# Kernel tuning notes

Hardware: AMD Instinct MI355X
Metric: run time of the kernel (lower is better)

Reference implementation:

```python
import jax, jax.numpy as jnp
import numpy as np

T, B, D, FF, Z = 1024, 32, 512, 2048, 64


def _trunc_normal(key, shape, std=0.001):
    return std * jax.random.truncated_normal(key, -2.0, 2.0, shape, dtype=jnp.float32)


def setup_inputs() -> dict:
    key = jax.random.key(0)
    ks = jax.random.split(key, 16)
    inp = {
        "x": jax.random.normal(ks[0], (T, B, D), dtype=jnp.float32),
        "first": jax.random.bernoulli(ks[1], 0.05, (T, B)),  # episode boundaries
        "h0": jax.random.normal(ks[2], (B, D), dtype=jnp.float32),
        "c0": jax.random.normal(ks[3], (B, D), dtype=jnp.float32),
        # pre-LN params
        "ln_g": jnp.ones((D,), jnp.float32),
        "ln_b": jnp.zeros((D,), jnp.float32),
        # LSTM params (PyTorch gate order i,f,g,o)
        "Wih": jax.random.normal(ks[4], (4 * D, D), jnp.float32) / np.sqrt(D),
        "Whh": jax.random.normal(ks[5], (4 * D, D), jnp.float32) / np.sqrt(D),
        "bih": jnp.zeros((4 * D,), jnp.float32),
        "bhh": jnp.zeros((4 * D,), jnp.float32),
        # pointwise FFN: mlp0 = Linear(D,FF)+ReLU, mlp1 = Linear(FF,D)
        "mlp0_w": jax.random.normal(ks[6], (FF, D), jnp.float32) / np.sqrt(D),
        "mlp0_b": jnp.zeros((FF,), jnp.float32),
        "mlp1_w": jax.random.normal(ks[7], (D, FF), jnp.float32) / np.sqrt(FF),
        "mlp1_b": jnp.zeros((D,), jnp.float32),
        # adapter bottleneck (trunc-normal init, std=0.001)
        "aw0": _trunc_normal(ks[8], (Z, D)),
        "ab0": _trunc_normal(ks[9], (Z,)),
        "aw1": _trunc_normal(ks[10], (D, Z)),
        "ab1": _trunc_normal(ks[11], (D,)),
    }
    return inp


def _layernorm(x, g, b, eps=1e-5):
    mu = jnp.mean(x, axis=-1, keepdims=True)
    var = jnp.mean(jnp.square(x - mu), axis=-1, keepdims=True)
    return (x - mu) * jax.lax.rsqrt(var + eps) * g + b


def _lstm_scan(x, first, h0, c0, Wih, Whh, bih, bhh):
    # x: [T,B,D], first: [T,B] bool resets state before the step
    def step(carry, inp):
        h, c = carry
        xt, ft = inp
        keep = jnp.where(ft, 0.0, 1.0)[:, None].astype(h.dtype)
        h = h * keep
        c = c * keep
        gates = xt @ Wih.T + bih + h @ Whh.T + bhh  # [B,4D]
        i, f, g, o = jnp.split(gates, 4, axis=-1)
        c = jax.nn.sigmoid(f) * c + jax.nn.sigmoid(i) * jnp.tanh(g)
        h = jax.nn.sigmoid(o) * jnp.tanh(c)
        return (h, c), h
    (h, c), ys = jax.lax.scan(step, (h0, c0), (x, first))
    return ys, h, c


def reference(x, first, h0, c0, ln_g, ln_b, Wih, Whh, bih, bhh,
              mlp0_w, mlp0_b, mlp1_w, mlp1_b, aw0, ab0, aw1, ab1):
    residual = x
    xn = _layernorm(x, ln_g, ln_b)
    y, h_out, c_out = _lstm_scan(xn, first, h0, c0, Wih, Whh, bih, bhh)
    y = y + residual  # is_residual and 'lstm' in recurrence_type
    residual = y
    # pointwise layer: mlp1(mlp0(y)) with mlp0 = Linear+ReLU
    y = jax.nn.relu(y @ mlp0_w.T + mlp0_b) @ mlp1_w.T + mlp1_b
    # adapter: y + net(y)
    y = y + jax.nn.relu(y @ aw0.T + ab0) @ aw1.T + ab1
    y = y + residual
    return (y, h_out, c_out)
```

## Files before the change

kernel.cpp:

```cpp
#include <hip/hip_runtime.h>

#define T_ 1024
#define B_ 32
#define D_ 512
#define FF_ 2048
#define TB_ 32768
#define TCH_ 512
#define RCH_ 16384

typedef short bf16x8 __attribute__((ext_vector_type(8)));
typedef float f32x4 __attribute__((ext_vector_type(4)));

static __device__ __forceinline__ unsigned int pack2bf(float a, float b){
  union { __bf16 h[2]; unsigned int u; } z;
  z.h[0] = (__bf16)a; z.h[1] = (__bf16)b; return z.u;
}
static __device__ __forceinline__ float bflo(unsigned int u){ return __uint_as_float(u<<16); }
static __device__ __forceinline__ float bfhi(unsigned int u){ return __uint_as_float(u & 0xffff0000u); }
static __device__ __forceinline__ float sigm(float x){ return 1.f/(1.f+__expf(-x)); }
static __device__ __forceinline__ float tanh_(float x){ return 1.f - 2.f/(1.f+__expf(2.f*x)); }

static __device__ __forceinline__ bool firstval(const void* p, int mode, int idx){
  return mode ? (((const int*)p)[idx] != 0) : (((const unsigned char*)p)[idx] != 0);
}

__global__ void detect_first_kernel(const unsigned char* __restrict__ p, unsigned int* __restrict__ mode){
  __shared__ int found;
  if (threadIdx.x == 0) found = 0;
  __syncthreads();
  int f = 0;
  for (int i = threadIdx.x; i < TB_; i += 256) if ((i & 3) != 0 && p[i] != 0) f = 1;
  if (f) atomicAdd(&found, 1);
  __syncthreads();
  if (threadIdx.x == 0) *mode = (found == 0) ? 1u : 0u;
}

__global__ void convert_w_kernel(const float* __restrict__ Wih, const float* __restrict__ Whh,
                                 const float* __restrict__ m0w, const float* __restrict__ m1w,
                                 const float* __restrict__ aw0, const float* __restrict__ aw1,
                                 __bf16* __restrict__ Wihb, __bf16* __restrict__ Whhb,
                                 __bf16* __restrict__ m0b,  __bf16* __restrict__ m1b,
                                 __bf16* __restrict__ awT0, __bf16* __restrict__ awT1){
  int bid = blockIdx.x;
  if (bid < 4096) {
    int ai = bid >> 10;
    size_t off = (size_t)(bid & 1023) * 1024 + threadIdx.x * 4;
    const float* src = (ai==0)?Wih:(ai==1)?Whh:(ai==2)?m0w:m1w;
    __bf16* dst = (ai==0)?Wihb:(ai==1)?Whhb:(ai==2)?m0b:m1b;
    float4 v = *(const float4*)(src + off);
    union { __bf16 h[4]; uint2 u; } z;
    z.h[0]=(__bf16)v.x; z.h[1]=(__bf16)v.y; z.h[2]=(__bf16)v.z; z.h[3]=(__bf16)v.w;
    *(uint2*)(void*)(dst + off) = z.u;
  } else {
    int e = (bid - 4096) * 256 + threadIdx.x;
    if (e < 32768) { int k = e >> 6, j = e & 63;  awT0[e] = (__bf16)aw0[j*512 + k]; }
    else { int e2 = e - 32768; int j = e2 >> 9, d = e2 & 511; awT1[e2] = (__bf16)aw1[d*64 + j]; }
  }
}

__global__ __launch_bounds__(256) void ln_kernel(const float* __restrict__ x,
                                                 const float* __restrict__ g, const float* __restrict__ b,
                                                 __bf16* __restrict__ xn){
  const int w = threadIdx.x >> 6, l = threadIdx.x & 63;
  const int row = blockIdx.x * 4 + w;
  const float* xr = x + (size_t)row * D_;
  const int e0 = l * 4, e1 = 256 + l * 4;
  float4 v0 = *(const float4*)(xr + e0);
  float4 v1 = *(const float4*)(xr + e1);
  float s  = v0.x+v0.y+v0.z+v0.w + v1.x+v1.y+v1.z+v1.w;
  float s2 = v0.x*v0.x+v0.y*v0.y+v0.z*v0.z+v0.w*v0.w + v1.x*v1.x+v1.y*v1.y+v1.z*v1.z+v1.w*v1.w;
  #pragma unroll
  for (int off = 1; off < 64; off <<= 1) { s += __shfl_xor(s, off); s2 += __shfl_xor(s2, off); }
  float mu = s * (1.f/512.f);
  float var = s2 * (1.f/512.f) - mu*mu;
  float rstd = rsqrtf(var + 1e-5f);
  float4 g0 = *(const float4*)(g + e0), g1 = *(const float4*)(g + e1);
  float4 b0 = *(const float4*)(b + e0), b1 = *(const float4*)(b + e1);
  union { __bf16 h[4]; uint2 u; } o0, o1;
  o0.h[0]=(__bf16)((v0.x-mu)*rstd*g0.x+b0.x); o0.h[1]=(__bf16)((v0.y-mu)*rstd*g0.y+b0.y);
  o0.h[2]=(__bf16)((v0.z-mu)*rstd*g0.z+b0.z); o0.h[3]=(__bf16)((v0.w-mu)*rstd*g0.w+b0.w);
  o1.h[0]=(__bf16)((v1.x-mu)*rstd*g1.x+b1.x); o1.h[1]=(__bf16)((v1.y-mu)*rstd*g1.y+b1.y);
  o1.h[2]=(__bf16)((v1.z-mu)*rstd*g1.z+b1.z); o1.h[3]=(__bf16)((v1.w-mu)*rstd*g1.w+b1.w);
  *(uint2*)(void*)(xn + (size_t)row * D_ + e0) = o0.u;
  *(uint2*)(void*)(xn + (size_t)row * D_ + e1) = o1.u;
}

template<int RELU, int BF16OUT, int TWOBIAS>
__global__ __launch_bounds__(256) void gemm_bt(const __bf16* __restrict__ A, const __bf16* __restrict__ W,
                                               const float* __restrict__ bias0, const float* __restrict__ bias1,
                                               float* __restrict__ Cf, __bf16* __restrict__ Cb,
                                               int M, int N, int K){
  __shared__ __bf16 As[128*64];
  __shared__ __bf16 Bs[128*64];
  const int tid = threadIdx.x, w = tid >> 6, l = tid & 63;
  const int bm = blockIdx.x, bn = blockIdx.y;
  const int wm = (w >> 1) * 64, wn = (w & 1) * 64;
  const int nk = K >> 6;

  uint4 ra[4], rb[4];
  #pragma unroll
  for (int i = 0; i < 4; ++i) {
    int s = tid + (i << 8); int row = s >> 3; int ks = s & 7;
    ra[i] = *(const uint4*)(void*)(A + (size_t)(bm*128 + row) * K + ks*8);
    rb[i] = *(const uint4*)(void*)(W + (size_t)(bn*128 + row) * K + ks*8);
  }
  f32x4 acc[4][4];
  #pragma unroll
  for (int mt = 0; mt < 4; ++mt)
    #pragma unroll
    for (int nt = 0; nt < 4; ++nt) acc[mt][nt] = (f32x4){0.f,0.f,0.f,0.f};

  for (int kt = 0; kt < nk; ++kt) {
    __syncthreads();
    #pragma unroll
    for (int i = 0; i < 4; ++i) {
      int s = tid + (i << 8); int row = s >> 3; int ks = s & 7;
      int wi = row * 64 + ((ks * 8) ^ ((row & 7) << 3));
      *(uint4*)(void*)(As + wi) = ra[i];
      *(uint4*)(void*)(Bs + wi) = rb[i];
    }
    __syncthreads();
    if (kt + 1 < nk) {
      #pragma unroll
      for (int i = 0; i < 4; ++i) {
        int s = tid + (i << 8); int row = s >> 3; int ks = s & 7;
        ra[i] = *(const uint4*)(void*)(A + (size_t)(bm*128 + row) * K + (kt+1)*64 + ks*8);
        rb[i] = *(const uint4*)(void*)(W + (size_t)(bn*128 + row) * K + (kt+1)*64 + ks*8);
      }
    }
    #pragma unroll
    for (int kk = 0; kk < 2; ++kk) {
      bf16x8 af[4], bfv[4];
      const int ke = kk * 32 + ((l >> 4) << 3);
      #pragma unroll
      for (int mt = 0; mt < 4; ++mt) {
        int row = wm + mt*16 + (l & 15);
        af[mt] = *(const bf16x8*)(void*)(As + row*64 + (ke ^ ((row & 7) << 3)));
      }
      #pragma unroll
      for (int nt = 0; nt < 4; ++nt) {
        int row = wn + nt*16 + (l & 15);
        bfv[nt] = *(const bf16x8*)(void*)(Bs + row*64 + (ke ^ ((row & 7) << 3)));
      }
      #pragma unroll
      for (int mt = 0; mt < 4; ++mt)
        #pragma unroll
        for (int nt = 0; nt < 4; ++nt)
          acc[mt][nt] = __builtin_amdgcn_mfma_f32_16x16x32_bf16(af[mt], bfv[nt], acc[mt][nt], 0, 0, 0);
    }
  }
  #pragma unroll
  for (int nt = 0; nt < 4; ++nt) {
    int c = bn*128 + wn + nt*16 + (l & 15);
    float bv = bias0[c];
    if (TWOBIAS) bv += bias1[c];
    #pragma unroll
    for (int mt = 0; mt < 4; ++mt) {
      #pragma unroll
      for (int j = 0; j < 4; ++j) {
        int r = bm*128 + wm + mt*16 + ((l >> 4) << 2) + j;
        float v = acc[mt][nt][j] + bv;
        if (RELU) v = fmaxf(v, 0.f);
        if (BF16OUT) Cb[(size_t)r * N + c] = (__bf16)v;
        else         Cf[(size_t)r * N + c] = v;
      }
    }
  }
}

__global__ __launch_bounds__(512) void lstm_scan(
    const __bf16* __restrict__ Whh,
    const __bf16* __restrict__ preC,
    const float*  __restrict__ x,
    const void*   __restrict__ firstp,
    const float*  __restrict__ h0,
    const float*  __restrict__ c0,
    float*        __restrict__ cstate,
    __bf16*       __restrict__ ymidbC,
    unsigned long long* __restrict__ HP,
    const unsigned int* __restrict__ modep,
    float* __restrict__ hout, float* __restrict__ cout,
    int tBase){
  const int s = blockIdx.x, tid = threadIdx.x, w = tid >> 6, l = tid & 63;
  const int d0 = s * 32;
  __shared__ __bf16 Hl[32 * 512];
  __shared__ float  gl[32 * 132];
  const int mode = (int)*modep;

  bf16x8 wf[16];
  {
    int rl = w*16 + (l & 15);
    int gr = (rl >> 5) * 512 + d0 + (rl & 31);
    const __bf16* base = Whh + (size_t)gr * 512 + ((l >> 4) << 3);
    #pragma unroll
    for (int kt = 0; kt < 16; ++kt) wf[kt] = *(const bf16x8*)(void*)(base + kt*32);
  }
  const int b = tid >> 4, dl2 = (tid & 15) * 2;
  const int dg = d0 + dl2;
  const int opid = b * 256 + s * 16 + (tid & 15);

  float cr[2];
  if (tBase == 0) {
    float k0 = firstval(firstp, mode, b) ? 0.f : 1.f;
    float2 c2 = *(const float2*)(c0 + (size_t)b*512 + dg);
    cr[0] = c2.x * k0; cr[1] = c2.y * k0;
    float2 h = *(const float2*)(h0 + (size_t)b*512 + dg);
    unsigned long long pkt = (1ULL << 32) | (unsigned long long)pack2bf(h.x*k0, h.y*k0);
    __hip_atomic_store(HP + opid, pkt, __ATOMIC_RELAXED, __HIP_MEMORY_SCOPE_AGENT);
  } else {
    float2 c2 = *(const float2*)(cstate + (size_t)b*512 + dg);
    cr[0] = c2.x; cr[1] = c2.y;
  }

  for (int tl = 0; tl < TCH_; ++tl) {
    const int t = tBase + tl;
    const int rowg = t * 32 + b, rowl = tl * 32 + b;
    unsigned int pg[4];
    #pragma unroll
    for (int gi = 0; gi < 4; ++gi)
      pg[gi] = *(const unsigned int*)(void*)(preC + (size_t)rowl * 2048 + gi*512 + dg);
    float2 xv = *(const float2*)(x + (size_t)rowg * 512 + dg);
    const bool f_t1 = (t < T_-1) ? firstval(firstp, mode, rowg + 32) : false;

    const unsigned want = (unsigned)(t + 1);
    const unsigned long long* Pb = HP + ((size_t)(t & 1) << 13);
    unsigned long long pk[16];
    #pragma unroll
    for (int j = 0; j < 16; ++j)
      pk[j] = __hip_atomic_load(Pb + tid + (j << 9), __ATOMIC_RELAXED, __HIP_MEMORY_SCOPE_AGENT);
    while (true) {
      unsigned stale = 0;
      #pragma unroll
      for (int j = 0; j < 16; ++j)
        if ((unsigned)(pk[j] >> 32) != want) stale |= (1u << j);
      if (!stale) break;
      __builtin_amdgcn_s_sleep(1);
      #pragma unroll
      for (int j = 0; j < 16; ++j)
        if (stale & (1u << j))
          pk[j] = __hip_atomic_load(Pb + tid + (j << 9), __ATOMIC_RELAXED, __HIP_MEMORY_SCOPE_AGENT);
    }
    #pragma unroll
    for (int j = 0; j < 16; ++j) {
      int pid = tid + (j << 9);
      int pb = pid >> 8, ps = (pid >> 4) & 15, pi = pid & 15;
      int q = ps*32 + pi*2;
      *(unsigned int*)(void*)(Hl + pb*512 + (q ^ ((pb & 7) << 3))) = (unsigned)pk[j];
    }
    __syncthreads();

    f32x4 a0a = (f32x4){0.f,0.f,0.f,0.f}, a0b = (f32x4){0.f,0.f,0.f,0.f};
    f32x4 a1a = (f32x4){0.f,0.f,0.f,0.f}, a1b = (f32x4){0.f,0.f,0.f,0.f};
    #pragma unroll
    for (int kt = 0; kt < 16; kt += 2) {
      int ke0 = kt*32 + ((l >> 4) << 3), ke1 = (kt+1)*32 + ((l >> 4) << 3);
      int r0 = (l & 15), r1 = 16 + (l & 15);
      bf16x8 h00 = *(const bf16x8*)(void*)(Hl + r0*512 + (ke0 ^ ((r0 & 7) << 3)));
      bf16x8 h01 = *(const bf16x8*)(void*)(Hl + r0*512 + (ke1 ^ ((r0 & 7) << 3)));
      bf16x8 h10 = *(const bf16x8*)(void*)(Hl + r1*512 + (ke0 ^ ((r1 & 7) << 3)));
      bf16x8 h11 = *(const bf16x8*)(void*)(Hl + r1*512 + (ke1 ^ ((r1 & 7) << 3)));
      a0a = __builtin_amdgcn_mfma_f32_16x16x32_bf16(h00, wf[kt],   a0a, 0, 0, 0);
      a0b = __builtin_amdgcn_mfma_f32_16x16x32_bf16(h01, wf[kt+1], a0b, 0, 0, 0);
      a1a = __builtin_amdgcn_mfma_f32_16x16x32_bf16(h10, wf[kt],   a1a, 0, 0, 0);
      a1b = __builtin_amdgcn_mfma_f32_16x16x32_bf16(h11, wf[kt+1], a1b, 0, 0, 0);
    }
    f32x4 acc0 = a0a + a0b, acc1 = a1a + a1b;
    {
      int col = w*16 + (l & 15);
      #pragma unroll
      for (int j = 0; j < 4; ++j) {
        gl[(((l >> 4) << 2) + j) * 132 + col]        = acc0[j];
        gl[((16 + ((l >> 4) << 2) + j)) * 132 + col] = acc1[j];
      }
    }
    __syncthreads();

    float2 gv[4];
    #pragma unroll
    for (int gi = 0; gi < 4; ++gi) gv[gi] = *(const float2*)(gl + b*132 + gi*32 + dl2);
    const float keep1 = f_t1 ? 0.f : 1.f;
    float hh[2], cc[2];
    #pragma unroll
    for (int p = 0; p < 2; ++p) {
      float gi_ = (p ? gv[0].y : gv[0].x) + (p ? bfhi(pg[0]) : bflo(pg[0]));
      float gf_ = (p ? gv[1].y : gv[1].x) + (p ? bfhi(pg[1]) : bflo(pg[1]));
      float gg_ = (p ? gv[2].y : gv[2].x) + (p ? bfhi(pg[2]) : bflo(pg[2]));
      float go_ = (p ? gv[3].y : gv[3].x) + (p ? bfhi(pg[3]) : bflo(pg[3]));
      float cn = sigm(gf_) * cr[p] + sigm(gi_) * tanh_(gg_);
      float h  = sigm(go_) * tanh_(cn);
      cc[p] = cn; hh[p] = h;
    }
    cr[0] = cc[0] * keep1; cr[1] = cc[1] * keep1;
    float2 yv = { hh[0] + xv.x, hh[1] + xv.y };
    if (t < T_-1) {
      unsigned long long pkt = (((unsigned long long)(unsigned)(t + 2)) << 32)
                             | (unsigned long long)pack2bf(hh[0]*keep1, hh[1]*keep1);
      __hip_atomic_store(HP + (((size_t)((t+1) & 1)) << 13) + opid, pkt,
                         __ATOMIC_RELAXED, __HIP_MEMORY_SCOPE_AGENT);
      if (tl == TCH_-1) *(float2*)(cstate + (size_t)b*512 + dg) = make_float2(cr[0], cr[1]);
    } else {
      *(float2*)(hout + (size_t)b*512 + dg) = make_float2(hh[0], hh[1]);
      *(float2*)(cout + (size_t)b*512 + dg) = make_float2(cc[0], cc[1]);
    }
    *(unsigned int*)(void*)(ymidbC + (size_t)rowl * 512 + dg) = pack2bf(yv.x, yv.y);
  }
}

__global__ __launch_bounds__(256) void adapter_out_kernel(
    float* __restrict__ y2,
    const __bf16* __restrict__ ymidb,
    const __bf16* __restrict__ awT0,
    const __bf16* __restrict__ awT1,
    const float* __restrict__ ab0, const float* __restrict__ ab1){
  __shared__ float zl[16 * 64];
  const int w = threadIdx.x >> 6, l = threadIdx.x & 63;
  const int r0 = blockIdx.x * 16;
  const float bz = ab0[l];
  #pragma unroll
  for (int rr = 0; rr < 4; ++rr) {
    int rowl = w*4 + rr;
    const float* yr = y2 + (size_t)(r0 + rowl) * 512;
    float acc = bz;
    #pragma unroll 4
    for (int k = 0; k < 512; ++k) acc += yr[k] * (float)awT0[k*64 + l];
    zl[rowl*64 + l] = fmaxf(acc, 0.f);
  }
  __syncthreads();
  #pragma unroll
  for (int rr = 0; rr < 4; ++rr) {
    int rowl = w*4 + rr; int row = r0 + rowl;
    const float* yr = y2  + (size_t)row * 512;
    const __bf16* mr = ymidb + (size_t)row * 512;
    #pragma unroll
    for (int dd = 0; dd < 8; ++dd) {
      int d = dd*64 + l;
      float acc = ab1[d] + yr[d] + (float)mr[d];
      #pragma unroll 4
      for (int j = 0; j < 64; ++j) acc += zl[rowl*64 + j] * (float)awT1[j*512 + d];
      y2[(size_t)row * 512 + d] = acc;
    }
  }
}

extern "C" void kernel_launch(void* const* d_in, const int* in_sizes, int n_in,
                              void* d_out, int out_size, void* d_ws, size_t ws_size,
                              hipStream_t stream){
  (void)in_sizes; (void)n_in; (void)out_size; (void)ws_size;
  const float* x    = (const float*)d_in[0];
  const void*  first=               d_in[1];
  const float* h0   = (const float*)d_in[2];
  const float* c0   = (const float*)d_in[3];
  const float* ln_g = (const float*)d_in[4];
  const float* ln_b = (const float*)d_in[5];
  const float* Wih  = (const float*)d_in[6];
  const float* Whh  = (const float*)d_in[7];
  const float* bih  = (const float*)d_in[8];
  const float* bhh  = (const float*)d_in[9];
  const float* m0w  = (const float*)d_in[10];
  const float* m0b  = (const float*)d_in[11];
  const float* m1w  = (const float*)d_in[12];
  const float* m1b  = (const float*)d_in[13];
  const float* aw0  = (const float*)d_in[14];
  const float* ab0  = (const float*)d_in[15];
  const float* aw1  = (const float*)d_in[16];
  const float* ab1  = (const float*)d_in[17];

  char* ws = (char*)d_ws;
  __bf16* buf0  = (__bf16*)(ws + 0LL);
  __bf16* xnbfH = (__bf16*)(ws + 67108864LL);
  __bf16* ymidbH= (__bf16*)(ws + 83886080LL);
  __bf16* wihb  = (__bf16*)(ws + 100663296LL);
  __bf16* whhb  = (__bf16*)(ws + 102760448LL);
  __bf16* m0bf  = (__bf16*)(ws + 104857600LL);
  __bf16* m1bf  = (__bf16*)(ws + 106954752LL);
  __bf16* awT0  = (__bf16*)(ws + 109051904LL);
  __bf16* awT1  = (__bf16*)(ws + 109117440LL);
  unsigned long long* HP = (unsigned long long*)(ws + 109182976LL);
  float*  cstate= (float*) (ws + 109314048LL);
  unsigned int* mode = (unsigned int*)(ws + 109379584LL);
  __bf16* preH = buf0;
  __bf16* a1   = buf0;

  float* out  = (float*)d_out;
  float* hout = out + (size_t)TB_ * D_;
  float* cout = hout + B_ * D_;

  hipMemsetAsync(HP, 0, 131072, stream);
  detect_first_kernel<<<1, 256, 0, stream>>>((const unsigned char*)first, mode);
  convert_w_kernel<<<4352, 256, 0, stream>>>(Wih, Whh, m0w, m1w, aw0, aw1,
                                             wihb, whhb, m0bf, m1bf, awT0, awT1);
  for (int h = 0; h < 2; ++h) {
    const size_t ro = (size_t)h * RCH_;
    ln_kernel<<<RCH_/4, 256, 0, stream>>>(x + ro * D_, ln_g, ln_b, xnbfH);
    gemm_bt<0,1,1><<<dim3(RCH_/128, FF_/128), 256, 0, stream>>>(xnbfH, wihb, bih, bhh,
                                                                nullptr, preH, RCH_, 2048, 512);
    lstm_scan<<<16, 512, 0, stream>>>(whhb, preH, x, first, h0, c0, cstate, ymidbH,
                                      HP, mode, hout, cout, h * TCH_);
    gemm_bt<1,1,0><<<dim3(RCH_/128, FF_/128), 256, 0, stream>>>(ymidbH, m0bf, m0b, nullptr,
                                                                nullptr, a1, RCH_, FF_, 512);
    gemm_bt<0,0,0><<<dim3(RCH_/128, D_/128), 256, 0, stream>>>(a1, m1bf, m1b, nullptr,
                                                               out + ro * D_, nullptr, RCH_, D_, FF_);
    adapter_out_kernel<<<RCH_/16, 256, 0, stream>>>(out + ro * D_, ymidbH, awT0, awT1, ab0, ab1);
  }
}
```

Before: 5.113 ms.

## Use direct global-to-LDS loads in GEMM and fp32 adapter weights

```diff
diff --git a/kernel.cpp b/kernel.cpp
--- a/kernel.cpp
+++ b/kernel.cpp
@@ -19,6 +19,12 @@
 static __device__ __forceinline__ float bfhi(unsigned int u){ return __uint_as_float(u & 0xffff0000u); }
 static __device__ __forceinline__ float sigm(float x){ return 1.f/(1.f+__expf(-x)); }
 static __device__ __forceinline__ float tanh_(float x){ return 1.f - 2.f/(1.f+__expf(2.f*x)); }
+
+static __device__ __forceinline__ void gload16(const __bf16* g, __bf16* l){
+  __builtin_amdgcn_global_load_lds(
+      (__attribute__((address_space(1))) const void*)g,
+      (__attribute__((address_space(3))) void*)l, 16, 0, 0);
+}
 
 static __device__ __forceinline__ bool firstval(const void* p, int mode, int idx){
   return mode ? (((const int*)p)[idx] != 0) : (((const unsigned char*)p)[idx] != 0);
@@ -40,7 +46,7 @@
                                  const float* __restrict__ aw0, const float* __restrict__ aw1,
                                  __bf16* __restrict__ Wihb, __bf16* __restrict__ Whhb,
                                  __bf16* __restrict__ m0b,  __bf16* __restrict__ m1b,
-                                 __bf16* __restrict__ awT0, __bf16* __restrict__ awT1){
+                                 float* __restrict__ awT0f, float* __restrict__ awT1f){
   int bid = blockIdx.x;
   if (bid < 4096) {
     int ai = bid >> 10;
@@ -53,8 +59,8 @@
     *(uint2*)(void*)(dst + off) = z.u;
   } else {
     int e = (bid - 4096) * 256 + threadIdx.x;
-    if (e < 32768) { int k = e >> 6, j = e & 63;  awT0[e] = (__bf16)aw0[j*512 + k]; }
-    else { int e2 = e - 32768; int j = e2 >> 9, d = e2 & 511; awT1[e2] = (__bf16)aw1[d*64 + j]; }
+    if (e < 32768) { int k = e >> 6, j = e & 63;  awT0f[e] = aw0[j*512 + k]; }
+    else { int e2 = e - 32768; int j = e2 >> 9, d = e2 & 511; awT1f[e2] = aw1[d*64 + j]; }
   }
 }
 
@@ -97,13 +103,14 @@
   const int wm = (w >> 1) * 64, wn = (w & 1) * 64;
   const int nk = K >> 6;
 
-  uint4 ra[4], rb[4];
+  int crow[4], ksrc[4];
   #pragma unroll
   for (int i = 0; i < 4; ++i) {
-    int s = tid + (i << 8); int row = s >> 3; int ks = s & 7;
-    ra[i] = *(const uint4*)(void*)(A + (size_t)(bm*128 + row) * K + ks*8);
-    rb[i] = *(const uint4*)(void*)(W + (size_t)(bn*128 + row) * K + ks*8);
-  }
+    int c = i*256 + w*64 + l;
+    crow[i] = c >> 3;
+    ksrc[i] = ((c & 7) * 8) ^ ((crow[i] & 7) << 3);
+  }
+
   f32x4 acc[4][4];
   #pragma unroll
   for (int mt = 0; mt < 4; ++mt)
@@ -111,23 +118,15 @@
     for (int nt = 0; nt < 4; ++nt) acc[mt][nt] = (f32x4){0.f,0.f,0.f,0.f};
 
   for (int kt = 0; kt < nk; ++kt) {
+    if (kt) __syncthreads();
+    #pragma unroll
+    for (int i = 0; i < 4; ++i) {
+      const __bf16* ga = A + (size_t)(bm*128 + crow[i]) * K + kt*64 + ksrc[i];
+      const __bf16* gb = W + (size_t)(bn*128 + crow[i]) * K + kt*64 + ksrc[i];
+      gload16(ga, As + (size_t)(i*256 + w*64) * 8);
+      gload16(gb, Bs + (size_t)(i*256 + w*64) * 8);
+    }
     __syncthreads();
-    #pragma unroll
-    for (int i = 0; i < 4; ++i) {
-      int s = tid + (i << 8); int row = s >> 3; int ks = s & 7;
-      int wi = row * 64 + ((ks * 8) ^ ((row & 7) << 3));
-      *(uint4*)(void*)(As + wi) = ra[i];
-      *(uint4*)(void*)(Bs + wi) = rb[i];
-    }
-    __syncthreads();
-    if (kt + 1 < nk) {
-      #pragma unroll
-      for (int i = 0; i < 4; ++i) {
-        int s = tid + (i << 8); int row = s >> 3; int ks = s & 7;
-        ra[i] = *(const uint4*)(void*)(A + (size_t)(bm*128 + row) * K + (kt+1)*64 + ks*8);
-        rb[i] = *(const uint4*)(void*)(W + (size_t)(bn*128 + row) * K + (kt+1)*64 + ks*8);
-      }
-    }
     #pragma unroll
     for (int kk = 0; kk < 2; ++kk) {
       bf16x8 af[4], bfv[4];
@@ -309,8 +308,8 @@
 __global__ __launch_bounds__(256) void adapter_out_kernel(
     float* __restrict__ y2,
     const __bf16* __restrict__ ymidb,
-    const __bf16* __restrict__ awT0,
-    const __bf16* __restrict__ awT1,
+    const float* __restrict__ awT0f,
+    const float* __restrict__ awT1f,
     const float* __restrict__ ab0, const float* __restrict__ ab1){
   __shared__ float zl[16 * 64];
   const int w = threadIdx.x >> 6, l = threadIdx.x & 63;
@@ -322,7 +321,11 @@
     const float* yr = y2 + (size_t)(r0 + rowl) * 512;
     float acc = bz;
     #pragma unroll 4
-    for (int k = 0; k < 512; ++k) acc += yr[k] * (float)awT0[k*64 + l];
+    for (int k = 0; k < 512; k += 4) {
+      float4 v = *(const float4*)(yr + k);
+      acc += v.x*awT0f[(k+0)*64 + l] + v.y*awT0f[(k+1)*64 + l]
+           + v.z*awT0f[(k+2)*64 + l] + v.w*awT0f[(k+3)*64 + l];
+    }
     zl[rowl*64 + l] = fmaxf(acc, 0.f);
   }
   __syncthreads();
@@ -336,7 +339,7 @@
       int d = dd*64 + l;
       float acc = ab1[d] + yr[d] + (float)mr[d];
       #pragma unroll 4
-      for (int j = 0; j < 64; ++j) acc += zl[rowl*64 + j] * (float)awT1[j*512 + d];
+      for (int j = 0; j < 64; ++j) acc += zl[rowl*64 + j] * awT1f[j*512 + d];
       y2[(size_t)row * 512 + d] = acc;
     }
   }
@@ -373,11 +376,11 @@
   __bf16* whhb  = (__bf16*)(ws + 102760448LL);
   __bf16* m0bf  = (__bf16*)(ws + 104857600LL);
   __bf16* m1bf  = (__bf16*)(ws + 106954752LL);
-  __bf16* awT0  = (__bf16*)(ws + 109051904LL);
-  __bf16* awT1  = (__bf16*)(ws + 109117440LL);
-  unsigned long long* HP = (unsigned long long*)(ws + 109182976LL);
-  float*  cstate= (float*) (ws + 109314048LL);
-  unsigned int* mode = (unsigned int*)(ws + 109379584LL);
+  float*  awT0f = (float*) (ws + 109051904LL);
+  float*  awT1f = (float*) (ws + 109182976LL);
+  unsigned long long* HP = (unsigned long long*)(ws + 109314048LL);
+  float*  cstate= (float*) (ws + 109445120LL);
+  unsigned int* mode = (unsigned int*)(ws + 109510656LL);
   __bf16* preH = buf0;
   __bf16* a1   = buf0;
 
@@ -388,7 +391,7 @@
   hipMemsetAsync(HP, 0, 131072, stream);
   detect_first_kernel<<<1, 256, 0, stream>>>((const unsigned char*)first, mode);
   convert_w_kernel<<<4352, 256, 0, stream>>>(Wih, Whh, m0w, m1w, aw0, aw1,
-                                             wihb, whhb, m0bf, m1bf, awT0, awT1);
+                                             wihb, whhb, m0bf, m1bf, awT0f, awT1f);
   for (int h = 0; h < 2; ++h) {
     const size_t ro = (size_t)h * RCH_;
     ln_kernel<<<RCH_/4, 256, 0, stream>>>(x + ro * D_, ln_g, ln_b, xnbfH);
@@ -400,6 +403,6 @@
                                                                 nullptr, a1, RCH_, FF_, 512);
     gemm_bt<0,0,0><<<dim3(RCH_/128, D_/128), 256, 0, stream>>>(a1, m1bf, m1b, nullptr,
                                                                out + ro * D_, nullptr, RCH_, D_, FF_);
-    adapter_out_kernel<<<RCH_/16, 256, 0, stream>>>(out + ro * D_, ymidbH, awT0, awT1, ab0, ab1);
-  }
-}
+    adapter_out_kernel<<<RCH_/16, 256, 0, stream>>>(out + ro * D_, ymidbH, awT0f, awT1f, ab0, ab1);
+  }
+}
```

New measurement: 4.377 ms. -14.4%, faster.
